# Kernel optimization log

Hardware: AMD Instinct MI355X
Metric: run time of the kernel (lower is better)

The kernel has to match this reference:

```python
import jax, jax.numpy as jnp
import numpy as np
import math

B, S, H = 2, 2048, 3072
NH, NKV, HD = 32, 32, 96
BASE = 10000.0
NEG = -1e9


def rotate_half(x):
    x1 = x[..., : x.shape[-1] // 2]
    x2 = x[..., x.shape[-1] // 2 :]
    return jnp.concatenate((-x2, x1), axis=-1)


def setup_inputs() -> dict:
    key = jax.random.key(0)
    k1, k2, k3 = jax.random.split(key, 3)
    hidden_states = jax.random.normal(k1, (B, S, H), dtype=jnp.float32)
    position_ids = jnp.broadcast_to(jnp.arange(S, dtype=jnp.int32), (B, S))
    # additive causal mask: 0 where key <= query, -1e9 above the diagonal
    i = jnp.arange(S)
    causal = jnp.where(i[None, :] <= i[:, None], 0.0, NEG).astype(jnp.float32)
    attention_mask = jnp.broadcast_to(causal[None, None], (B, 1, S, S))
    w_qkv = jax.random.normal(k2, (NH * HD + 2 * NKV * HD, H), dtype=jnp.float32) * 0.02
    w_o = jax.random.normal(k3, (H, NH * HD), dtype=jnp.float32) * 0.02
    return {
        "hidden_states": hidden_states,
        "position_ids": position_ids,
        "attention_mask": attention_mask,
        "w_qkv": w_qkv,
        "w_o": w_o,
    }


def reference(hidden_states, position_ids, attention_mask, w_qkv, w_o):
    bsz, q_len, _ = hidden_states.shape
    # fused QKV projection (no bias), then split per Phi3 layout
    qkv = jnp.einsum("bsh,oh->bso", hidden_states, w_qkv)
    q = qkv[..., : NH * HD]
    k = qkv[..., NH * HD : NH * HD + NKV * HD]
    v = qkv[..., NH * HD + NKV * HD :]
    q = q.reshape(bsz, q_len, NH, HD).transpose(0, 2, 1, 3)   # [B,NH,S,HD]
    k = k.reshape(bsz, q_len, NKV, HD).transpose(0, 2, 1, 3)  # [B,NKV,S,HD]
    v = v.reshape(bsz, q_len, NKV, HD).transpose(0, 2, 1, 3)

    # rotary embeddings (Phi3RotaryEmbedding, no scaling)
    inv_freq = 1.0 / (BASE ** (jnp.arange(0, HD, 2, dtype=jnp.float32) / HD))  # [HD/2]
    freqs = position_ids.astype(jnp.float32)[:, :, None] * inv_freq[None, None, :]  # [B,S,HD/2]
    emb = jnp.concatenate((freqs, freqs), axis=-1)  # [B,S,HD]
    cos = jnp.cos(emb)[:, None].astype(hidden_states.dtype)  # [B,1,S,HD]
    sin = jnp.sin(emb)[:, None].astype(hidden_states.dtype)
    q = q * cos + rotate_half(q) * sin
    k = k * cos + rotate_half(k) * sin
    # num_key_value_groups = NH // NKV = 1 -> repeat_kv is a no-op

    attn = jnp.einsum("bhqd,bhkd->bhqk", q, k) / math.sqrt(HD)
    attn = attn + attention_mask  # broadcast over heads
    attn = jax.nn.softmax(attn.astype(jnp.float32), axis=-1).astype(v.dtype)
    # attention_dropout = 0.0 / eval mode -> dropout is identity
    out = jnp.einsum("bhqk,bhkd->bhqd", attn, v)
    out = out.transpose(0, 2, 1, 3).reshape(bsz, q_len, NH * HD)
    return jnp.einsum("bso,ho->bsh", out, w_o)
```

## Files before the change

kernel.cpp:

```cpp
#include <hip/hip_runtime.h>
#include <hip/hip_bf16.h>
#include <type_traits>

typedef unsigned short ushort_t;
typedef __attribute__((ext_vector_type(8))) short bf16x8;
typedef __attribute__((ext_vector_type(4))) float f32x4;

#define S_LEN 2048
#define NHEAD 32
#define HDIM 96

__device__ __forceinline__ float bf2f(ushort_t b) {
    union { unsigned u; float f; } v; v.u = ((unsigned)b) << 16; return v.f;
}
__device__ __forceinline__ ushort_t f2bf(float f) {
    union { float f; unsigned u; } v; v.f = f;
    unsigned r = v.u + 0x7fffu + ((v.u >> 16) & 1u);
    return (ushort_t)(r >> 16);
}
__device__ __forceinline__ void cp16(ushort_t* l, const ushort_t* g) {
    __builtin_amdgcn_global_load_lds((const __attribute__((address_space(1))) void*)g,
                                     (__attribute__((address_space(3))) void*)l, 16, 0, 0);
}

__global__ void cvt_f32_bf16(const float* __restrict__ src, ushort_t* __restrict__ dst, int n8)
{
    const int i = blockIdx.x * 256 + threadIdx.x;
    if (i >= n8) return;
    const float4 a = ((const float4*)src)[2 * i];
    const float4 b = ((const float4*)src)[2 * i + 1];
    union { ushort_t us[8]; int4 v; } r;
    r.us[0] = f2bf(a.x); r.us[1] = f2bf(a.y); r.us[2] = f2bf(a.z); r.us[3] = f2bf(a.w);
    r.us[4] = f2bf(b.x); r.us[5] = f2bf(b.y); r.us[6] = f2bf(b.z); r.us[7] = f2bf(b.w);
    ((int4*)dst)[i] = r.v;
}

template <typename OT>
__global__ __launch_bounds__(512, 2) void gemm256(
    const ushort_t* __restrict__ A, const ushort_t* __restrict__ Bm,
    OT* __restrict__ C, int M, int N, int K)
{
    __shared__ ushort_t As[2][16384];
    __shared__ ushort_t Bs[2][12288];
    const int tid = threadIdx.x;
    const int lane = tid & 63, w = tid >> 6;
    const int wm = w >> 2, wn = w & 3;
    const int r16 = lane & 15, quad = lane >> 4;

    const int m0 = blockIdx.y * 256;
    const int n0 = blockIdx.x * 192;

    const int sl8 = ((tid & 3) ^ ((tid >> 3) & 3)) * 8;
    const int srow = tid >> 2;
    const ushort_t* gA  = A  + (size_t)(m0 + srow) * K + sl8;
    const size_t rsk = (size_t)128 * K;
    const ushort_t* gB0 = Bm + (size_t)(n0 + srow) * K + sl8;
    const ushort_t* gB1 = Bm + (size_t)(n0 + ((tid < 256) ? (128 + srow) : ((tid - 256) >> 2))) * K
                          + ((tid < 256) ? 0 : 32) + sl8;
    const ushort_t* gB2 = Bm + (size_t)(n0 + 64 + srow) * K + 32 + sl8;

    const int laneoff = r16 * 32 + (quad ^ ((r16 >> 1) & 3)) * 8;

    f32x4 acc[8][3];
#pragma unroll
    for (int m = 0; m < 8; m++)
#pragma unroll
        for (int j = 0; j < 3; j++) acc[m][j] = f32x4{0.f, 0.f, 0.f, 0.f};

    const int NT = K >> 6;

#define STAGE_B(bn, kb)  { cp16(&Bs[bn][tid * 8],         gB0 + (kb)); \
                           cp16(&Bs[bn][tid * 8 + 4096],  gB1 + (kb)); \
                           cp16(&Bs[bn][tid * 8 + 8192],  gB2 + (kb)); }
#define STAGE_A0(bn, kb) { cp16(&As[bn][tid * 8],         gA + (kb)); \
                           cp16(&As[bn][tid * 8 + 4096],  gA + rsk + (kb)); }
#define STAGE_A1(bn, kb) { cp16(&As[bn][tid * 8 + 8192],  gA + (kb) + 32); \
                           cp16(&As[bn][tid * 8 + 12288], gA + rsk + (kb) + 32); }

    STAGE_B(0, 0);
    STAGE_A0(0, 0);
    STAGE_A1(0, 0);
    asm volatile("s_waitcnt vmcnt(2)" ::: "memory");
    __builtin_amdgcn_s_barrier();

    for (int t = 0; t < NT; ++t) {
        const int b = t & 1, bn = b ^ 1;
        const int kb = (t + 1) << 6;
        bf16x8 av[8], bv[3];

#pragma unroll
        for (int j = 0; j < 3; j++)
            bv[j] = *(const bf16x8*)&Bs[b][(wn * 48 + j * 16) * 32 + laneoff];
#pragma unroll
        for (int m = 0; m < 8; m++)
            av[m] = *(const bf16x8*)&As[b][(wm * 128 + m * 16) * 32 + laneoff];
        if (t + 1 < NT) {
            STAGE_B(bn, kb);
            STAGE_A0(bn, kb);
        }
        __builtin_amdgcn_s_barrier();
        __builtin_amdgcn_s_setprio(1);
#pragma unroll
        for (int m = 0; m < 8; m++)
#pragma unroll
            for (int j = 0; j < 3; j++)
                acc[m][j] = __builtin_amdgcn_mfma_f32_16x16x32_bf16(av[m], bv[j], acc[m][j], 0, 0, 0);
        __builtin_amdgcn_s_setprio(0);
        if (t + 1 < NT) {
            asm volatile("s_waitcnt vmcnt(5)" ::: "memory");
        } else {
            asm volatile("s_waitcnt vmcnt(0)" ::: "memory");
        }
        __builtin_amdgcn_s_barrier();

#pragma unroll
        for (int j = 0; j < 3; j++)
            bv[j] = *(const bf16x8*)&Bs[b][6144 + (wn * 48 + j * 16) * 32 + laneoff];
#pragma unroll
        for (int m = 0; m < 8; m++)
            av[m] = *(const bf16x8*)&As[b][8192 + (wm * 128 + m * 16) * 32 + laneoff];
        if (t + 1 < NT) {
            STAGE_A1(bn, kb);
        }
        __builtin_amdgcn_s_barrier();
        __builtin_amdgcn_s_setprio(1);
#pragma unroll
        for (int m = 0; m < 8; m++)
#pragma unroll
            for (int j = 0; j < 3; j++)
                acc[m][j] = __builtin_amdgcn_mfma_f32_16x16x32_bf16(av[m], bv[j], acc[m][j], 0, 0, 0);
        __builtin_amdgcn_s_setprio(0);
        asm volatile("s_waitcnt vmcnt(2)" ::: "memory");
        __builtin_amdgcn_s_barrier();
    }
#undef STAGE_B
#undef STAGE_A0
#undef STAGE_A1

#pragma unroll
    for (int m = 0; m < 8; m++) {
        const int row0 = m0 + wm * 128 + m * 16 + quad * 4;
#pragma unroll
        for (int j = 0; j < 3; j++) {
            const int col = n0 + wn * 48 + j * 16 + r16;
#pragma unroll
            for (int r = 0; r < 4; r++) {
                if constexpr (std::is_same<OT, float>::value)
                    C[(size_t)(row0 + r) * N + col] = acc[m][j][r];
                else
                    C[(size_t)(row0 + r) * N + col] = f2bf(acc[m][j][r]);
            }
        }
    }
}

__global__ void rope_scatter(const ushort_t* __restrict__ qkv, const int* __restrict__ pos,
                             ushort_t* __restrict__ Q, ushort_t* __restrict__ Kd)
{
    const int d = threadIdx.x;
    const int t = blockIdx.x * 2 + threadIdx.y;
    const int h = blockIdx.y;
    const int which = d >= 48;
    const int dd = which ? d - 48 : d;
    const int p = pos[t];
    const float inv = exp2f((float)dd * (-13.287712379549449f / 48.0f));
    const float th = (float)p * inv;
    const float cs = cosf(th), sn = sinf(th);
    const ushort_t* src = qkv + (size_t)t * 9216 + (which ? 3072 : 0) + h * 96;
    const float x1 = bf2f(src[dd]), x2 = bf2f(src[dd + 48]);
    ushort_t* dst = (which ? Kd : Q) +
        ((size_t)((t >> 11) * NHEAD + h) * S_LEN + (t & 2047)) * HDIM;
    dst[dd]      = f2bf(x1 * cs - x2 * sn);
    dst[dd + 48] = f2bf(x2 * cs + x1 * sn);
}

__global__ void v_transpose(const ushort_t* __restrict__ qkv, ushort_t* __restrict__ VT)
{
    const int t = blockIdx.x * 64 + threadIdx.x;
    const int h = blockIdx.y;
    const int d = blockIdx.z * 8 + threadIdx.y;
    const int b = t >> 11, s = t & 2047;
    VT[((size_t)(b * NHEAD + h) * HDIM + d) * S_LEN + s] =
        qkv[(size_t)t * 9216 + 6144 + h * 96 + d];
}

__global__ __launch_bounds__(256, 2) void flash_attn(
    const ushort_t* __restrict__ Q, const ushort_t* __restrict__ Kg,
    const ushort_t* __restrict__ VT, ushort_t* __restrict__ attn)
{
    __shared__ ushort_t Qs[128 * 104];
    __shared__ ushort_t Ps[128 * 72];

    const int tid = threadIdx.x, w = tid >> 6, lane = tid & 63;
    const int r16 = lane & 15, quad = lane >> 4;
    const int qi = 15 - (blockIdx.x >> 6);
    const int bh = blockIdx.x & 63;
    const int q0 = qi * 128;
    const ushort_t* Qg  = Q  + ((size_t)bh * S_LEN + q0) * HDIM;
    const ushort_t* Kgb = Kg + (size_t)bh * S_LEN * HDIM;
    const ushort_t* Vgb = VT + (size_t)bh * HDIM * S_LEN;

#pragma unroll
    for (int c = 0; c < 6; c++) {
        const int cc = tid + 256 * c;
        const int row = cc / 12, col = (cc % 12) * 8;
        *(int4*)&Qs[row * 104 + col] = *(const int4*)(Qg + row * 96 + col);
    }
    __syncthreads();

    float m_st[2][4], l_st[2][4];
#pragma unroll
    for (int i = 0; i < 2; i++)
#pragma unroll
        for (int r = 0; r < 4; r++) { m_st[i][r] = -1.0e30f; l_st[i][r] = 0.f; }

    f32x4 o[2][6];
#pragma unroll
    for (int i = 0; i < 2; i++)
#pragma unroll
        for (int jo = 0; jo < 6; jo++) o[i][jo] = f32x4{0.f, 0.f, 0.f, 0.f};

    const float sc = 0.10206207261596577f;
    const float L2E = 1.4426950408889634f;
    const int nkt = 2 * qi + 2;
    const int rowb = 32 * w;

    for (int kt = 0; kt < nkt; ++kt) {
        const int k0 = kt * 64;

        f32x4 sacc[2][4];
#pragma unroll
        for (int i = 0; i < 2; i++)
#pragma unroll
            for (int j = 0; j < 4; j++) sacc[i][j] = f32x4{0.f, 0.f, 0.f, 0.f};
#pragma unroll
        for (int kk = 0; kk < 3; kk++) {
            bf16x8 qa[2], kb[4];
#pragma unroll
            for (int i = 0; i < 2; i++)
                qa[i] = *(const bf16x8*)&Qs[(rowb + 16 * i + r16) * 104 + kk * 32 + quad * 8];
#pragma unroll
            for (int j = 0; j < 4; j++)
                kb[j] = *(const bf16x8*)(Kgb + (size_t)(k0 + 16 * j + r16) * 96
                                         + kk * 32 + quad * 8);
#pragma unroll
            for (int i = 0; i < 2; i++)
#pragma unroll
                for (int j = 0; j < 4; j++)
                    sacc[i][j] = __builtin_amdgcn_mfma_f32_16x16x32_bf16(qa[i], kb[j], sacc[i][j], 0, 0, 0);
        }

        const bool need_mask = (kt >= 2 * qi);
#pragma unroll
        for (int i = 0; i < 2; i++)
#pragma unroll
            for (int j = 0; j < 4; j++)
#pragma unroll
                for (int r = 0; r < 4; r++) {
                    float v = sacc[i][j][r] * sc;
                    if (need_mask) {
                        const int grow = q0 + rowb + 16 * i + quad * 4 + r;
                        const int gcol = k0 + 16 * j + r16;
                        if (gcol > grow) v = -1.0e9f;
                    }
                    sacc[i][j][r] = v;
                }

        float mt[2][4];
#pragma unroll
        for (int i = 0; i < 2; i++)
#pragma unroll
            for (int r = 0; r < 4; r++) {
                float mp = fmaxf(fmaxf(sacc[i][0][r], sacc[i][1][r]),
                                 fmaxf(sacc[i][2][r], sacc[i][3][r]));
                mp = fmaxf(mp, __shfl_xor(mp, 1, 16));
                mp = fmaxf(mp, __shfl_xor(mp, 2, 16));
                mp = fmaxf(mp, __shfl_xor(mp, 4, 16));
                mp = fmaxf(mp, __shfl_xor(mp, 8, 16));
                mt[i][r] = mp;
            }

        float alpha[2][4];
#pragma unroll
        for (int i = 0; i < 2; i++)
#pragma unroll
            for (int r = 0; r < 4; r++) {
                const float mn = fmaxf(m_st[i][r], mt[i][r]);
                alpha[i][r] = exp2f((m_st[i][r] - mn) * L2E);
                m_st[i][r] = mn;
            }

        float psum[2][4];
#pragma unroll
        for (int i = 0; i < 2; i++)
#pragma unroll
            for (int r = 0; r < 4; r++) psum[i][r] = 0.f;
#pragma unroll
        for (int i = 0; i < 2; i++)
#pragma unroll
            for (int j = 0; j < 4; j++)
#pragma unroll
                for (int r = 0; r < 4; r++) {
                    const float p = exp2f((sacc[i][j][r] - m_st[i][r]) * L2E);
                    psum[i][r] += p;
                    Ps[(rowb + 16 * i + quad * 4 + r) * 72 + 16 * j + r16] = f2bf(p);
                }
#pragma unroll
        for (int i = 0; i < 2; i++)
#pragma unroll
            for (int r = 0; r < 4; r++) {
                float s2 = psum[i][r];
                s2 += __shfl_xor(s2, 1, 16);
                s2 += __shfl_xor(s2, 2, 16);
                s2 += __shfl_xor(s2, 4, 16);
                s2 += __shfl_xor(s2, 8, 16);
                l_st[i][r] = l_st[i][r] * alpha[i][r] + s2;
            }

#pragma unroll
        for (int i = 0; i < 2; i++)
#pragma unroll
            for (int jo = 0; jo < 6; jo++)
#pragma unroll
                for (int r = 0; r < 4; r++) o[i][jo][r] *= alpha[i][r];
#pragma unroll
        for (int kk = 0; kk < 2; kk++) {
            bf16x8 pa[2], vb[6];
#pragma unroll
            for (int i = 0; i < 2; i++)
                pa[i] = *(const bf16x8*)&Ps[(rowb + 16 * i + r16) * 72 + kk * 32 + quad * 8];
#pragma unroll
            for (int jo = 0; jo < 6; jo++)
                vb[jo] = *(const bf16x8*)(Vgb + (size_t)(16 * jo + r16) * S_LEN
                                          + k0 + kk * 32 + quad * 8);
#pragma unroll
            for (int i = 0; i < 2; i++)
#pragma unroll
                for (int jo = 0; jo < 6; jo++)
                    o[i][jo] = __builtin_amdgcn_mfma_f32_16x16x32_bf16(pa[i], vb[jo], o[i][jo], 0, 0, 0);
        }
    }

    const int b = bh >> 5, h = bh & 31;
#pragma unroll
    for (int i = 0; i < 2; i++)
#pragma unroll
        for (int r = 0; r < 4; r++) {
            const int lr = rowb + 16 * i + quad * 4 + r;
            const float inv = 1.0f / l_st[i][r];
            const size_t base = (size_t)(b * S_LEN + q0 + lr) * 3072 + h * 96;
#pragma unroll
            for (int jo = 0; jo < 6; jo++)
                attn[base + 16 * jo + r16] = f2bf(o[i][jo][r] * inv);
        }
}

extern "C" void kernel_launch(void* const* d_in, const int* in_sizes, int n_in,
                              void* d_out, int out_size, void* d_ws, size_t ws_size,
                              hipStream_t stream)
{
    const float* hidden = (const float*)d_in[0];
    const int*   pos    = (const int*)d_in[1];
    const float* w_qkv  = (const float*)d_in[3];
    const float* w_o    = (const float*)d_in[4];
    float* out          = (float*)d_out;

    char* ws = (char*)d_ws;
    ushort_t* hbf    = (ushort_t*)(ws);
    ushort_t* wqkvbf = (ushort_t*)(ws + 25165824);
    ushort_t* Qb     = (ushort_t*)(ws);
    ushort_t* Kb     = (ushort_t*)(ws + 25165824);
    ushort_t* VTb    = (ushort_t*)(ws + 50331648);
    ushort_t* qkv    = (ushort_t*)(ws + 81788928);
    ushort_t* attn   = qkv;
    ushort_t* wobf   = (ushort_t*)(ws + 157286400);

    cvt_f32_bf16<<<dim3(12582912 / 8 / 256), 256, 0, stream>>>(hidden, hbf, 12582912 / 8);
    cvt_f32_bf16<<<dim3(28311552 / 8 / 256), 256, 0, stream>>>(w_qkv, wqkvbf, 28311552 / 8);
    cvt_f32_bf16<<<dim3(9437184 / 8 / 256), 256, 0, stream>>>(w_o, wobf, 9437184 / 8);

    gemm256<ushort_t><<<dim3(48, 16), 512, 0, stream>>>(hbf, wqkvbf, qkv, 4096, 9216, 3072);
    rope_scatter<<<dim3(2048, 32), dim3(96, 2), 0, stream>>>(qkv, pos, Qb, Kb);
    v_transpose<<<dim3(64, 32, 12), dim3(64, 8), 0, stream>>>(qkv, VTb);
    flash_attn<<<dim3(1024), 256, 0, stream>>>(Qb, Kb, VTb, attn);
    gemm256<float><<<dim3(16, 16), 512, 0, stream>>>(attn, wobf, out, 4096, 3072, 3072);
}
```

Before: 846.1 us.

## Add 256x288-tile QKV GEMM and LDS-tiled V transpose

Replaces the QKV projection GEMM with a new kernel that uses 256x288 tiles and 768 threads (12 waves in a 2x6 grid). This gives 512 blocks, down from 768, which is meant to improve wave balance across CUs and reuse of A tiles. It also replaces the naive strided V transpose with an LDS-staged tile transpose, so the writes to VT become coalesced. The larger tile raises LDS use to about 136KB per block and register pressure, which may limit occupancy despite the launch bound of 3.

```diff
diff --git a/kernel.cpp b/kernel.cpp
--- a/kernel.cpp
+++ b/kernel.cpp
@@ -33,6 +33,129 @@
     r.us[0] = f2bf(a.x); r.us[1] = f2bf(a.y); r.us[2] = f2bf(a.z); r.us[3] = f2bf(a.w);
     r.us[4] = f2bf(b.x); r.us[5] = f2bf(b.y); r.us[6] = f2bf(b.z); r.us[7] = f2bf(b.w);
     ((int4*)dst)[i] = r.v;
+}
+
+__global__ __launch_bounds__(768, 3) void gemm288(
+    const ushort_t* __restrict__ A, const ushort_t* __restrict__ Bm,
+    ushort_t* __restrict__ C, int M, int N, int K)
+{
+    __shared__ ushort_t As[2][16384];
+    __shared__ ushort_t Bs[2][18432];
+    const int tid = threadIdx.x;
+    const int lane = tid & 63, w = tid >> 6;
+    const int wm = w / 6, wn = w % 6;
+    const int r16 = lane & 15, quad = lane >> 4;
+
+    const int m0 = blockIdx.y * 256;
+    const int n0 = blockIdx.x * 288;
+
+    const ushort_t* gp[3];
+    ushort_t* lp[3];
+    int bstr[3], pstr[3];
+#pragma unroll
+    for (int j = 0; j < 3; j++) {
+        int c = tid + 768 * j;
+        if (c >= 2176) c -= 2176;
+        if (c < 1024) {
+            const int row = c >> 2;
+            gp[j] = A + (size_t)(m0 + row) * K + (((c & 3) ^ ((row >> 1) & 3)) * 8);
+            lp[j] = &As[0][c * 8];
+            bstr[j] = 16384; pstr[j] = 8192;
+        } else {
+            const int cb = c - 1024;
+            const int row = cb >> 2;
+            gp[j] = Bm + (size_t)(n0 + row) * K + (((cb & 3) ^ ((row >> 1) & 3)) * 8);
+            lp[j] = &Bs[0][cb * 8];
+            bstr[j] = 18432; pstr[j] = 9216;
+        }
+    }
+#define STAGE(buf, ks, ko) { \
+    cp16(lp[0] + (buf) * bstr[0] + (ks) * pstr[0], gp[0] + (ko) + (ks) * 32); \
+    cp16(lp[1] + (buf) * bstr[1] + (ks) * pstr[1], gp[1] + (ko) + (ks) * 32); \
+    cp16(lp[2] + (buf) * bstr[2] + (ks) * pstr[2], gp[2] + (ko) + (ks) * 32); }
+
+    const int laneoff = r16 * 32 + (quad ^ ((r16 >> 1) & 3)) * 8;
+
+    f32x4 acc[8][3];
+#pragma unroll
+    for (int m = 0; m < 8; m++)
+#pragma unroll
+        for (int j = 0; j < 3; j++) acc[m][j] = f32x4{0.f, 0.f, 0.f, 0.f};
+
+    const int NT = K >> 6;
+
+    STAGE(0, 0, 0);
+    STAGE(0, 1, 0);
+    asm volatile("s_waitcnt vmcnt(3)" ::: "memory");
+    __builtin_amdgcn_s_barrier();
+    asm volatile("" ::: "memory");
+
+    for (int t = 0; t < NT; ++t) {
+        const int b = t & 1, bn = b ^ 1;
+        const int ko = (t + 1) << 6;
+        bf16x8 av[8], bv[3];
+
+#pragma unroll
+        for (int j = 0; j < 3; j++)
+            bv[j] = *(const bf16x8*)&Bs[b][(wn * 48 + j * 16) * 32 + laneoff];
+#pragma unroll
+        for (int m = 0; m < 8; m++)
+            av[m] = *(const bf16x8*)&As[b][(wm * 128 + m * 16) * 32 + laneoff];
+        if (t + 1 < NT) STAGE(bn, 0, ko);
+        __builtin_amdgcn_s_barrier();
+        asm volatile("" ::: "memory");
+        __builtin_amdgcn_s_setprio(1);
+#pragma unroll
+        for (int m = 0; m < 8; m++)
+#pragma unroll
+            for (int j = 0; j < 3; j++)
+                acc[m][j] = __builtin_amdgcn_mfma_f32_16x16x32_bf16(av[m], bv[j], acc[m][j], 0, 0, 0);
+        __builtin_amdgcn_s_setprio(0);
+        if (t + 1 < NT) {
+            asm volatile("s_waitcnt vmcnt(3)" ::: "memory");
+        } else {
+            asm volatile("s_waitcnt vmcnt(0)" ::: "memory");
+        }
+        __builtin_amdgcn_s_barrier();
+        asm volatile("" ::: "memory");
+
+#pragma unroll
+        for (int j = 0; j < 3; j++)
+            bv[j] = *(const bf16x8*)&Bs[b][9216 + (wn * 48 + j * 16) * 32 + laneoff];
+#pragma unroll
+        for (int m = 0; m < 8; m++)
+            av[m] = *(const bf16x8*)&As[b][8192 + (wm * 128 + m * 16) * 32 + laneoff];
+        if (t + 1 < NT) STAGE(bn, 1, ko);
+        __builtin_amdgcn_s_barrier();
+        asm volatile("" ::: "memory");
+        __builtin_amdgcn_s_setprio(1);
+#pragma unroll
+        for (int m = 0; m < 8; m++)
+#pragma unroll
+            for (int j = 0; j < 3; j++)
+                acc[m][j] = __builtin_amdgcn_mfma_f32_16x16x32_bf16(av[m], bv[j], acc[m][j], 0, 0, 0);
+        __builtin_amdgcn_s_setprio(0);
+        if (t + 1 < NT) {
+            asm volatile("s_waitcnt vmcnt(3)" ::: "memory");
+        } else {
+            asm volatile("s_waitcnt vmcnt(0)" ::: "memory");
+        }
+        __builtin_amdgcn_s_barrier();
+        asm volatile("" ::: "memory");
+    }
+#undef STAGE
+
+#pragma unroll
+    for (int m = 0; m < 8; m++) {
+        const int row0 = m0 + wm * 128 + m * 16 + quad * 4;
+#pragma unroll
+        for (int j = 0; j < 3; j++) {
+            const int col = n0 + wn * 48 + j * 16 + r16;
+#pragma unroll
+            for (int r = 0; r < 4; r++)
+                C[(size_t)(row0 + r) * N + col] = f2bf(acc[m][j][r]);
+        }
+    }
 }
 
 template <typename OT>
@@ -174,14 +297,29 @@
     dst[dd + 48] = f2bf(x2 * cs + x1 * sn);
 }
 
-__global__ void v_transpose(const ushort_t* __restrict__ qkv, ushort_t* __restrict__ VT)
-{
-    const int t = blockIdx.x * 64 + threadIdx.x;
-    const int h = blockIdx.y;
-    const int d = blockIdx.z * 8 + threadIdx.y;
-    const int b = t >> 11, s = t & 2047;
-    VT[((size_t)(b * NHEAD + h) * HDIM + d) * S_LEN + s] =
-        qkv[(size_t)t * 9216 + 6144 + h * 96 + d];
+__global__ __launch_bounds__(256) void v_transpose2(const ushort_t* __restrict__ qkv,
+                                                    ushort_t* __restrict__ VT)
+{
+    __shared__ ushort_t tl[64 * 102];
+    const int tid = threadIdx.x;
+    const int s0 = blockIdx.x * 64;
+    const int h  = blockIdx.y;
+    const int b  = blockIdx.z;
+    const ushort_t* src = qkv + ((size_t)(b * 2048 + s0)) * 9216 + 6144 + h * 96;
+#pragma unroll
+    for (int k = 0; k < 24; k++) {
+        const int idx = tid + 256 * k;
+        const int r = idx / 96, c = idx % 96;
+        tl[r * 102 + c] = src[(size_t)r * 9216 + c];
+    }
+    __syncthreads();
+    ushort_t* dst = VT + (size_t)(b * NHEAD + h) * HDIM * S_LEN + s0;
+#pragma unroll
+    for (int k = 0; k < 24; k++) {
+        const int idx = tid + 256 * k;
+        const int d = idx >> 6, s = idx & 63;
+        dst[(size_t)d * S_LEN + s] = tl[s * 102 + d];
+    }
 }
 
 __global__ __launch_bounds__(256, 2) void flash_attn(
@@ -379,9 +517,9 @@
     cvt_f32_bf16<<<dim3(28311552 / 8 / 256), 256, 0, stream>>>(w_qkv, wqkvbf, 28311552 / 8);
     cvt_f32_bf16<<<dim3(9437184 / 8 / 256), 256, 0, stream>>>(w_o, wobf, 9437184 / 8);
 
-    gemm256<ushort_t><<<dim3(48, 16), 512, 0, stream>>>(hbf, wqkvbf, qkv, 4096, 9216, 3072);
+    gemm288<<<dim3(32, 16), 768, 0, stream>>>(hbf, wqkvbf, qkv, 4096, 9216, 3072);
     rope_scatter<<<dim3(2048, 32), dim3(96, 2), 0, stream>>>(qkv, pos, Qb, Kb);
-    v_transpose<<<dim3(64, 32, 12), dim3(64, 8), 0, stream>>>(qkv, VTb);
+    v_transpose2<<<dim3(32, 32, 2), 256, 0, stream>>>(qkv, VTb);
     flash_attn<<<dim3(1024), 256, 0, stream>>>(Qb, Kb, VTb, attn);
     gemm256<float><<<dim3(16, 16), 512, 0, stream>>>(attn, wobf, out, 4096, 3072, 3072);
 }
```

Result: faster. 737.5 us (-12.8%).
